# Performance work log

Hardware: AMD Instinct MI355X
Metric: run time of the kernel (lower is better)

## Reference

```python
import jax, jax.numpy as jnp
import numpy as np

B, N, INDIM, OUTDIM = 32, 128, 32, 64


def setup_inputs() -> dict:
    key = jax.random.key(0)
    k1, k2, k3, k4, k5, k6 = jax.random.split(key, 6)
    X = jax.random.normal(k1, (B, N, N, INDIM), dtype=jnp.float32)
    # variable subgraph sizes (irregular masking), at least 1 node per graph
    n_nodes = jnp.clip(jax.random.randint(k2, (B,), 0, N), 1, N).astype(jnp.int64)
    # MLP params (Linear + ReLU tail activation) for lin1 and lin2
    s = 1.0 / np.sqrt(INDIM)
    W1 = jax.random.uniform(k3, (INDIM, OUTDIM), jnp.float32, -s, s)
    b1 = jax.random.uniform(k4, (OUTDIM,), jnp.float32, -s, s)
    W2 = jax.random.uniform(k5, (INDIM, OUTDIM), jnp.float32, -s, s)
    b2 = jax.random.uniform(k6, (OUTDIM,), jnp.float32, -s, s)
    return {"X": X, "W1": W1, "b1": b1, "W2": W2, "b2": b2, "n_nodes": n_nodes}


def reference(X, W1, b1, W2, b2, n_nodes):
    # pairwise mask [B,N,N,1] from per-graph node counts (MaskedTensor mode 'DD')
    nm = jnp.arange(N)[None, :] < n_nodes[:, None]          # [B,N] node mask
    mask = (nm[:, :, None] & nm[:, None, :])[..., None].astype(X.dtype)  # [B,N,N,1]
    # tuplewiseapply of lin1 / lin2 (Linear + ReLU), zero-fill masked tuples
    X1 = jax.nn.relu(jnp.einsum('bijd,de->bije', X, W1) + b1) * mask  # [B,N,N,OUTDIM]
    X2 = jax.nn.relu(jnp.einsum('bijd,de->bije', X, W2) + b2) * mask
    # Op2FWL (aggr='sum'): per-channel batched matmul over node dim k
    out = jnp.einsum('bike,bkje->bije', X1, X2) * mask
    return out
```

## Files before the change

kernel.cpp:

```cpp
#include <hip/hip_runtime.h>

typedef unsigned short ushort_t;
typedef __attribute__((ext_vector_type(8))) __bf16 bf16x8;
typedef __attribute__((ext_vector_type(4))) float f32x4;


__device__ __forceinline__ ushort_t f32_to_bf16(float v) {
    unsigned ui = __float_as_uint(v);
    ui += 0x7fffu + ((ui >> 16) & 1u);
    return (ushort_t)(ui >> 16);
}

union FragU { bf16x8 f; ushort_t u[8]; };
union Pack4 { ushort_t us[4]; uint2 v; };

__global__ __launch_bounds__(256) void lin_mfma_kernel(
        const float* __restrict__ X, const float* __restrict__ W,
        const float* __restrict__ bias, const int* __restrict__ n_nodes,
        ushort_t* __restrict__ Out, int rstride, int tstride) {
    __shared__ ushort_t sO[64 * 136];
    const int blk = blockIdx.x;
    const int b = blk >> 7, r = blk & 127;
    const float* Xb = X + (size_t)b * 524288 + (size_t)r * rstride;
    const int u = threadIdx.x;
    const int w = u >> 6, l = u & 63;
    const int quad = l >> 4, lid = l & 15;
    const int n = n_nodes[b];
    const bool rin = (r < n);

    FragU bfrag[4];
    float bia[4];
    #pragma unroll
    for (int ni = 0; ni < 4; ++ni) {
        const int e = ni * 16 + lid;
        #pragma unroll
        for (int j = 0; j < 8; ++j)
            bfrag[ni].u[j] = f32_to_bf16(W[(quad * 8 + j) * 64 + e]);
        bia[ni] = bias[e];
    }

    #pragma unroll
    for (int s = 0; s < 2; ++s) {
        const int mt = w * 2 + s;
        const int m = mt * 16 + lid;
        const float* xr = Xb + (size_t)m * tstride + quad * 8;
        float4 x0 = *(const float4*)xr;
        float4 x1 = *(const float4*)(xr + 4);
        FragU af;
        af.u[0] = f32_to_bf16(x0.x); af.u[1] = f32_to_bf16(x0.y);
        af.u[2] = f32_to_bf16(x0.z); af.u[3] = f32_to_bf16(x0.w);
        af.u[4] = f32_to_bf16(x1.x); af.u[5] = f32_to_bf16(x1.y);
        af.u[6] = f32_to_bf16(x1.z); af.u[7] = f32_to_bf16(x1.w);

        #pragma unroll
        for (int ni = 0; ni < 4; ++ni) {
            f32x4 acc = {};
            acc = __builtin_amdgcn_mfma_f32_16x16x32_bf16(af.f, bfrag[ni].f, acc, 0, 0, 0);
            const int e = ni * 16 + lid;
            const int t0 = mt * 16 + quad * 4;
            Pack4 pk;
            #pragma unroll
            for (int rg = 0; rg < 4; ++rg) {
                const int t = t0 + rg;
                float v = (rin && t < n) ? fmaxf(acc[rg] + bia[ni], 0.f) : 0.f;
                pk.us[rg] = f32_to_bf16(v);
            }
            *(uint2*)(sO + e * 136 + t0) = pk.v;
        }
    }
    __syncthreads();
    {
        const int e = u >> 2, part = u & 3;
        ushort_t* gO = Out + ((size_t)(b * 64 + e) * 128 + r) * 128 + part * 32;
        const ushort_t* sRow = sO + e * 136 + part * 32;
        #pragma unroll
        for (int c = 0; c < 4; ++c)
            *(uint4*)(gO + c * 8) = *(const uint4*)(sRow + c * 8);
    }
}

__global__ __launch_bounds__(256) void mm_kernel(
        const ushort_t* __restrict__ X1t, const ushort_t* __restrict__ X2t,
        ushort_t* __restrict__ Ct) {
    __shared__ ushort_t sC[128 * 136];
    const int blk = blockIdx.x;
    const size_t plane = (size_t)blk * 16384;
    const ushort_t* Aj = X2t + plane;
    const ushort_t* Bi = X1t + plane;
    const int u = threadIdx.x;
    const int w = u >> 6, l = u & 63;
    const int quad = l >> 4, lid = l & 15;
    const int wj = (w >> 1) * 64, wi = (w & 1) * 64;
    f32x4 acc[4][4] = {};

    #pragma unroll
    for (int k0 = 0; k0 < 128; k0 += 32) {
        bf16x8 af[4], bfr[4];
        #pragma unroll
        for (int mj = 0; mj < 4; ++mj)
            af[mj] = *(const bf16x8*)(Aj + (size_t)(wj + mj * 16 + lid) * 128 + k0 + quad * 8);
        #pragma unroll
        for (int ni = 0; ni < 4; ++ni)
            bfr[ni] = *(const bf16x8*)(Bi + (size_t)(wi + ni * 16 + lid) * 128 + k0 + quad * 8);
        #pragma unroll
        for (int mj = 0; mj < 4; ++mj)
            #pragma unroll
            for (int ni = 0; ni < 4; ++ni)
                acc[mj][ni] = __builtin_amdgcn_mfma_f32_16x16x32_bf16(
                    af[mj], bfr[ni], acc[mj][ni], 0, 0, 0);
    }

    #pragma unroll
    for (int mj = 0; mj < 4; ++mj)
        #pragma unroll
        for (int ni = 0; ni < 4; ++ni) {
            const int j0 = wj + mj * 16 + quad * 4;
            const int i  = wi + ni * 16 + lid;
            Pack4 pk;
            #pragma unroll
            for (int rg = 0; rg < 4; ++rg)
                pk.us[rg] = f32_to_bf16(acc[mj][ni][rg]);
            *(uint2*)(sC + i * 136 + j0) = pk.v;
        }
    __syncthreads();
    ushort_t* Cp = Ct + plane;
    #pragma unroll
    for (int it = 0; it < 8; ++it) {
        int idx = it * 256 + u;
        int i = idx >> 4, c = idx & 15;
        *(uint4*)(Cp + (size_t)idx * 8) = *(const uint4*)(sC + i * 136 + c * 8);
    }
}

__global__ __launch_bounds__(256) void tr_kernel(
        const ushort_t* __restrict__ Ct, float* __restrict__ out) {
    __shared__ float sT[64 * 129];
    const int blk = blockIdx.x;
    const int b = blk >> 7, i = blk & 127;
    const int u = threadIdx.x;
    const ushort_t* Cb = Ct + (size_t)b * 1048576 + (size_t)i * 128;

    #pragma unroll
    for (int it = 0; it < 4; ++it) {
        int idx = it * 256 + u;
        int e = idx >> 4, c = idx & 15;
        uint4 v = *(const uint4*)(Cb + (size_t)e * 16384 + c * 8);
        float* dst = sT + e * 129 + c * 8;
        dst[0] = __uint_as_float(v.x << 16);
        dst[1] = __uint_as_float(v.x & 0xffff0000u);
        dst[2] = __uint_as_float(v.y << 16);
        dst[3] = __uint_as_float(v.y & 0xffff0000u);
        dst[4] = __uint_as_float(v.z << 16);
        dst[5] = __uint_as_float(v.z & 0xffff0000u);
        dst[6] = __uint_as_float(v.w << 16);
        dst[7] = __uint_as_float(v.w & 0xffff0000u);
    }
    __syncthreads();

    float* ob = out + ((size_t)b * 16384 + (size_t)i * 128) * 64;
    #pragma unroll
    for (int it = 0; it < 8; ++it) {
        int idx = it * 256 + u;
        int j = idx >> 4, e0 = (idx & 15) * 4;
        float4 vv;
        vv.x = sT[(e0 + 0) * 129 + j];
        vv.y = sT[(e0 + 1) * 129 + j];
        vv.z = sT[(e0 + 2) * 129 + j];
        vv.w = sT[(e0 + 3) * 129 + j];
        *(float4*)(ob + (size_t)idx * 4) = vv;
    }
}

extern "C" void kernel_launch(void* const* d_in, const int* in_sizes, int n_in,
                              void* d_out, int out_size, void* d_ws, size_t ws_size,
                              hipStream_t stream) {
    const float* X  = (const float*)d_in[0];
    const float* W1 = (const float*)d_in[1];
    const float* b1 = (const float*)d_in[2];
    const float* W2 = (const float*)d_in[3];
    const float* b2 = (const float*)d_in[4];
    const int* nn   = (const int*)d_in[5];
    float* out = (float*)d_out;

    ushort_t* X1t = (ushort_t*)d_ws;
    ushort_t* X2t = X1t + 33554432;
    ushort_t* Ct  = X1t;

    lin_mfma_kernel<<<4096, 256, 0, stream>>>(X, W1, b1, nn, X1t, 4096, 32);
    lin_mfma_kernel<<<4096, 256, 0, stream>>>(X, W2, b2, nn, X2t, 32, 4096);
    mm_kernel<<<2048, 256, 0, stream>>>(X1t, X2t, Ct);
    tr_kernel<<<4096, 256, 0, stream>>>(Ct, out);
}
```

Measured before the change: 286.0 us.

## Skip masked rows, tiles and K-chunks using per-graph node counts

Uses n_nodes to skip work for out-of-range nodes in all three stages. The linear stage now runs both projections in one launch, with each block handling four rows. It skips X reads and MFMAs for masked rows and tiles and writes zeros instead. The batched matmul limits its K loop to the rounded-up node count and skips MFMA tiles and fragment loads outside the active region. The transpose kernel writes zeros directly for masked rows and skips reading masked columns. Since node counts are random, this is meant to cut much of the memory traffic and compute, at the cost of extra branching, less unrolling and load imbalance between blocks.

```diff
diff --git a/kernel.cpp b/kernel.cpp
--- a/kernel.cpp
+++ b/kernel.cpp
@@ -15,18 +15,26 @@
 union Pack4 { ushort_t us[4]; uint2 v; };
 
 __global__ __launch_bounds__(256) void lin_mfma_kernel(
-        const float* __restrict__ X, const float* __restrict__ W,
-        const float* __restrict__ bias, const int* __restrict__ n_nodes,
-        ushort_t* __restrict__ Out, int rstride, int tstride) {
+        const float* __restrict__ X,
+        const float* __restrict__ W1, const float* __restrict__ b1v,
+        const float* __restrict__ W2, const float* __restrict__ b2v,
+        const int* __restrict__ n_nodes,
+        ushort_t* __restrict__ X1t, ushort_t* __restrict__ X2t) {
     __shared__ ushort_t sO[64 * 136];
     const int blk = blockIdx.x;
-    const int b = blk >> 7, r = blk & 127;
-    const float* Xb = X + (size_t)b * 524288 + (size_t)r * rstride;
+    const int pass = blk >> 10;
+    const int idx = blk & 1023;
+    const int b = idx >> 5, rg = idx & 31;
+    const float* W    = pass ? W2  : W1;
+    const float* bias = pass ? b2v : b1v;
+    ushort_t* Out     = pass ? X2t : X1t;
+    const int rstride = pass ? 32 : 4096;
+    const int tstride = pass ? 4096 : 32;
+
     const int u = threadIdx.x;
     const int w = u >> 6, l = u & 63;
     const int quad = l >> 4, lid = l & 15;
     const int n = n_nodes[b];
-    const bool rin = (r < n);
 
     FragU bfrag[4];
     float bia[4];
@@ -39,75 +47,107 @@
         bia[ni] = bias[e];
     }
 
-    #pragma unroll
-    for (int s = 0; s < 2; ++s) {
-        const int mt = w * 2 + s;
-        const int m = mt * 16 + lid;
-        const float* xr = Xb + (size_t)m * tstride + quad * 8;
-        float4 x0 = *(const float4*)xr;
-        float4 x1 = *(const float4*)(xr + 4);
-        FragU af;
-        af.u[0] = f32_to_bf16(x0.x); af.u[1] = f32_to_bf16(x0.y);
-        af.u[2] = f32_to_bf16(x0.z); af.u[3] = f32_to_bf16(x0.w);
-        af.u[4] = f32_to_bf16(x1.x); af.u[5] = f32_to_bf16(x1.y);
-        af.u[6] = f32_to_bf16(x1.z); af.u[7] = f32_to_bf16(x1.w);
-
-        #pragma unroll
-        for (int ni = 0; ni < 4; ++ni) {
-            f32x4 acc = {};
-            acc = __builtin_amdgcn_mfma_f32_16x16x32_bf16(af.f, bfrag[ni].f, acc, 0, 0, 0);
-            const int e = ni * 16 + lid;
-            const int t0 = mt * 16 + quad * 4;
-            Pack4 pk;
-            #pragma unroll
-            for (int rg = 0; rg < 4; ++rg) {
-                const int t = t0 + rg;
-                float v = (rin && t < n) ? fmaxf(acc[rg] + bia[ni], 0.f) : 0.f;
-                pk.us[rg] = f32_to_bf16(v);
+    for (int q = 0; q < 4; ++q) {
+        const int r = rg * 4 + q;
+        const bool rin = (r < n);
+        if (rin) {
+            const float* Xb = X + (size_t)b * 524288 + (size_t)r * rstride;
+            #pragma unroll
+            for (int s = 0; s < 2; ++s) {
+                const int mt = w * 2 + s;
+                const int t0b = mt * 16 + quad * 4;
+                if (mt * 16 < n) {
+                    const int m = mt * 16 + lid;
+                    const float* xr = Xb + (size_t)m * tstride + quad * 8;
+                    float4 x0 = *(const float4*)xr;
+                    float4 x1 = *(const float4*)(xr + 4);
+                    FragU af;
+                    af.u[0] = f32_to_bf16(x0.x); af.u[1] = f32_to_bf16(x0.y);
+                    af.u[2] = f32_to_bf16(x0.z); af.u[3] = f32_to_bf16(x0.w);
+                    af.u[4] = f32_to_bf16(x1.x); af.u[5] = f32_to_bf16(x1.y);
+                    af.u[6] = f32_to_bf16(x1.z); af.u[7] = f32_to_bf16(x1.w);
+                    #pragma unroll
+                    for (int ni = 0; ni < 4; ++ni) {
+                        f32x4 acc = {};
+                        acc = __builtin_amdgcn_mfma_f32_16x16x32_bf16(
+                            af.f, bfrag[ni].f, acc, 0, 0, 0);
+                        const int e = ni * 16 + lid;
+                        Pack4 pk;
+                        #pragma unroll
+                        for (int rgi = 0; rgi < 4; ++rgi) {
+                            const int t = t0b + rgi;
+                            float v = (t < n) ? fmaxf(acc[rgi] + bia[ni], 0.f) : 0.f;
+                            pk.us[rgi] = f32_to_bf16(v);
+                        }
+                        *(uint2*)(sO + e * 136 + t0b) = pk.v;
+                    }
+                } else {
+                    Pack4 pk; pk.us[0] = pk.us[1] = pk.us[2] = pk.us[3] = 0;
+                    #pragma unroll
+                    for (int ni = 0; ni < 4; ++ni)
+                        *(uint2*)(sO + (ni * 16 + lid) * 136 + t0b) = pk.v;
+                }
             }
-            *(uint2*)(sO + e * 136 + t0) = pk.v;
-        }
-    }
-    __syncthreads();
-    {
-        const int e = u >> 2, part = u & 3;
-        ushort_t* gO = Out + ((size_t)(b * 64 + e) * 128 + r) * 128 + part * 32;
-        const ushort_t* sRow = sO + e * 136 + part * 32;
-        #pragma unroll
-        for (int c = 0; c < 4; ++c)
-            *(uint4*)(gO + c * 8) = *(const uint4*)(sRow + c * 8);
+        }
+        __syncthreads();
+        {
+            const int e = u >> 2, part = u & 3;
+            ushort_t* gO = Out + ((size_t)(b * 64 + e) * 128 + r) * 128 + part * 32;
+            if (rin) {
+                const ushort_t* sRow = sO + e * 136 + part * 32;
+                #pragma unroll
+                for (int c = 0; c < 4; ++c)
+                    *(uint4*)(gO + c * 8) = *(const uint4*)(sRow + c * 8);
+            } else {
+                uint4 z = {0, 0, 0, 0};
+                #pragma unroll
+                for (int c = 0; c < 4; ++c)
+                    *(uint4*)(gO + c * 8) = z;
+            }
+        }
+        __syncthreads();
     }
 }
 
 __global__ __launch_bounds__(256) void mm_kernel(
         const ushort_t* __restrict__ X1t, const ushort_t* __restrict__ X2t,
-        ushort_t* __restrict__ Ct) {
+        ushort_t* __restrict__ Ct, const int* __restrict__ n_nodes) {
     __shared__ ushort_t sC[128 * 136];
     const int blk = blockIdx.x;
     const size_t plane = (size_t)blk * 16384;
+    const int n = n_nodes[blk >> 6];
+    const int kmax = (n + 31) & ~31;
     const ushort_t* Aj = X2t + plane;
     const ushort_t* Bi = X1t + plane;
     const int u = threadIdx.x;
     const int w = u >> 6, l = u & 63;
     const int quad = l >> 4, lid = l & 15;
     const int wj = (w >> 1) * 64, wi = (w & 1) * 64;
+    const bool anyA = (wj < n), anyB = (wi < n);
+    bool aAct[4], bAct[4];
+    #pragma unroll
+    for (int mj = 0; mj < 4; ++mj) aAct[mj] = (wj + mj * 16) < n;
+    #pragma unroll
+    for (int ni = 0; ni < 4; ++ni) bAct[ni] = (wi + ni * 16) < n;
     f32x4 acc[4][4] = {};
 
-    #pragma unroll
-    for (int k0 = 0; k0 < 128; k0 += 32) {
+    for (int k0 = 0; k0 < kmax; k0 += 32) {
         bf16x8 af[4], bfr[4];
         #pragma unroll
         for (int mj = 0; mj < 4; ++mj)
-            af[mj] = *(const bf16x8*)(Aj + (size_t)(wj + mj * 16 + lid) * 128 + k0 + quad * 8);
+            if (aAct[mj] && anyB)
+                af[mj] = *(const bf16x8*)(Aj + (size_t)(wj + mj * 16 + lid) * 128 + k0 + quad * 8);
         #pragma unroll
         for (int ni = 0; ni < 4; ++ni)
-            bfr[ni] = *(const bf16x8*)(Bi + (size_t)(wi + ni * 16 + lid) * 128 + k0 + quad * 8);
+            if (bAct[ni] && anyA)
+                bfr[ni] = *(const bf16x8*)(Bi + (size_t)(wi + ni * 16 + lid) * 128 + k0 + quad * 8);
         #pragma unroll
         for (int mj = 0; mj < 4; ++mj)
             #pragma unroll
             for (int ni = 0; ni < 4; ++ni)
-                acc[mj][ni] = __builtin_amdgcn_mfma_f32_16x16x32_bf16(
-                    af[mj], bfr[ni], acc[mj][ni], 0, 0, 0);
+                if (aAct[mj] && bAct[ni])
+                    acc[mj][ni] = __builtin_amdgcn_mfma_f32_16x16x32_bf16(
+                        af[mj], bfr[ni], acc[mj][ni], 0, 0, 0);
     }
 
     #pragma unroll
@@ -133,31 +173,46 @@
 }
 
 __global__ __launch_bounds__(256) void tr_kernel(
-        const ushort_t* __restrict__ Ct, float* __restrict__ out) {
+        const ushort_t* __restrict__ Ct, float* __restrict__ out,
+        const int* __restrict__ n_nodes) {
     __shared__ float sT[64 * 129];
     const int blk = blockIdx.x;
     const int b = blk >> 7, i = blk & 127;
     const int u = threadIdx.x;
+    const int n = n_nodes[b];
+    float* ob = out + ((size_t)b * 16384 + (size_t)i * 128) * 64;
+
+    if (i >= n) {
+        float4 z = {0.f, 0.f, 0.f, 0.f};
+        #pragma unroll
+        for (int it = 0; it < 8; ++it)
+            *(float4*)(ob + (size_t)(it * 256 + u) * 4) = z;
+        return;
+    }
+
     const ushort_t* Cb = Ct + (size_t)b * 1048576 + (size_t)i * 128;
-
     #pragma unroll
     for (int it = 0; it < 4; ++it) {
         int idx = it * 256 + u;
         int e = idx >> 4, c = idx & 15;
-        uint4 v = *(const uint4*)(Cb + (size_t)e * 16384 + c * 8);
         float* dst = sT + e * 129 + c * 8;
-        dst[0] = __uint_as_float(v.x << 16);
-        dst[1] = __uint_as_float(v.x & 0xffff0000u);
-        dst[2] = __uint_as_float(v.y << 16);
-        dst[3] = __uint_as_float(v.y & 0xffff0000u);
-        dst[4] = __uint_as_float(v.z << 16);
-        dst[5] = __uint_as_float(v.z & 0xffff0000u);
-        dst[6] = __uint_as_float(v.w << 16);
-        dst[7] = __uint_as_float(v.w & 0xffff0000u);
+        if (c * 8 < n) {
+            uint4 v = *(const uint4*)(Cb + (size_t)e * 16384 + c * 8);
+            dst[0] = __uint_as_float(v.x << 16);
+            dst[1] = __uint_as_float(v.x & 0xffff0000u);
+            dst[2] = __uint_as_float(v.y << 16);
+            dst[3] = __uint_as_float(v.y & 0xffff0000u);
+            dst[4] = __uint_as_float(v.z << 16);
+            dst[5] = __uint_as_float(v.z & 0xffff0000u);
+            dst[6] = __uint_as_float(v.w << 16);
+            dst[7] = __uint_as_float(v.w & 0xffff0000u);
+        } else {
+            #pragma unroll
+            for (int t = 0; t < 8; ++t) dst[t] = 0.f;
+        }
     }
     __syncthreads();
 
-    float* ob = out + ((size_t)b * 16384 + (size_t)i * 128) * 64;
     #pragma unroll
     for (int it = 0; it < 8; ++it) {
         int idx = it * 256 + u;
@@ -186,8 +241,7 @@
     ushort_t* X2t = X1t + 33554432;
     ushort_t* Ct  = X1t;
 
-    lin_mfma_kernel<<<4096, 256, 0, stream>>>(X, W1, b1, nn, X1t, 4096, 32);
-    lin_mfma_kernel<<<4096, 256, 0, stream>>>(X, W2, b2, nn, X2t, 32, 4096);
-    mm_kernel<<<2048, 256, 0, stream>>>(X1t, X2t, Ct);
-    tr_kernel<<<4096, 256, 0, stream>>>(Ct, out);
-}
+    lin_mfma_kernel<<<2048, 256, 0, stream>>>(X, W1, b1, W2, b2, nn, X1t, X2t);
+    mm_kernel<<<2048, 256, 0, stream>>>(X1t, X2t, Ct, nn);
+    tr_kernel<<<4096, 256, 0, stream>>>(Ct, out, nn);
+}
```

Result: faster. 270.5 us (-5.4%).
